# Performance work log

Hardware: AMD Instinct MI355X
Metric: run time of the kernel (lower is better)

Reference implementation:

```python
import jax, jax.numpy as jnp
import numpy as np

DIM = 64
B_GRAPHS = 16
N_NODES = 4096
N_EDGES = 16384
SLOPE = 0.01  # PyTorch leaky_relu default negative slope


def lrelu(x):
    return jnp.where(x >= 0, x, SLOPE * x)


def setup_inputs() -> dict:
    key = jax.random.key(0)
    ks = jax.random.split(key, 16)
    d = DIM

    def rn(k, shape, scale=0.05):
        return jax.random.normal(k, shape, dtype=jnp.float32) * scale

    def z(*s):
        return jnp.zeros(s, jnp.float32)

    return {
        "x": jax.random.normal(ks[0], (N_NODES, 3), dtype=jnp.float32),
        "edge_attr": jax.random.normal(ks[1], (N_EDGES, 4), dtype=jnp.float32),
        "edge_index": jax.random.randint(ks[2], (2, N_EDGES), 0, N_NODES),
        "batch": jnp.sort(jax.random.randint(ks[3], (N_NODES,), 0, B_GRAPHS)),
        # lin0
        "W0": rn(ks[4], (3, d)), "b0": z(d),
        # edge MLP: Linear(4,d) -> LeakyReLU -> Linear(d, d*d)
        "We1": rn(ks[5], (4, d)), "be1": z(d),
        "We2": rn(ks[6], (d, d * d), 0.01), "be2": z(d * d),
        # NNConv root weight + bias
        "root": rn(ks[7], (d, d)), "conv_b": z(d),
        # GRU(d, d)  (PyTorch layout: [3d, in] / [3d, hid], gate order r,z,n)
        "Wih": rn(ks[8], (3 * d, d)), "Whh": rn(ks[9], (3 * d, d)),
        "bih": z(3 * d), "bhh": z(3 * d),
        # Set2Set LSTM(2d, d)  (gate order i,f,g,o)
        "lWih": rn(ks[10], (4 * d, 2 * d)), "lWhh": rn(ks[11], (4 * d, d)),
        "lbih": z(4 * d), "lbhh": z(4 * d),
        # lin_out: Linear(2d, 2)
        "Wout": rn(ks[12], (2 * d, 2)), "bout": z(2),
    }


def _forward(x, edge_attr, W0, b0, We1, be1, We2, be2, root, conv_b,
             Wih, Whh, bih, bhh, lWih, lWhh, lbih, lbhh, Wout, bout,
             edge_index, batch):
    d = DIM
    N = x.shape[0]
    E = edge_attr.shape[0]
    src, dst = edge_index[0], edge_index[1]  # messages flow src(j) -> dst(i)

    out = lrelu(x @ W0 + b0)  # [N, d]
    h = out                    # GRU hidden state (h = out.unsqueeze(0))

    # Edge-conditioned weights: constant across the 6 iterations, compute once.
    he = lrelu(edge_attr @ We1 + be1)          # [E, d]
    W_e = (he @ We2 + be2).reshape(E, d, d)    # [E, d, d]
    deg = jax.ops.segment_sum(jnp.ones((E,), jnp.float32), dst, num_segments=N)
    inv_deg = (1.0 / jnp.maximum(deg, 1.0))[:, None]  # mean aggr, clamp like PyG

    for _ in range(6):
        # NNConv: gather x_j, per-edge matmul, scatter-mean, plus root term
        msg = jnp.einsum('ed,edf->ef', out[src], W_e)            # [E, d]
        agg = jax.ops.segment_sum(msg, dst, num_segments=N) * inv_deg
        m = lrelu(agg + out @ root + conv_b)                     # [N, d]
        # GRU cell (single step, PyTorch gate order r, z, n)
        gi = m @ Wih.T + bih
        gh = h @ Whh.T + bhh
        i_r, i_z, i_n = jnp.split(gi, 3, axis=-1)
        h_r, h_z, h_n = jnp.split(gh, 3, axis=-1)
        r = jax.nn.sigmoid(i_r + h_r)
        zg = jax.nn.sigmoid(i_z + h_z)
        n = jnp.tanh(i_n + r * h_n)
        h = (1.0 - zg) * n + zg * h
        out = h

    # Set2Set pooling, processing_steps = 1
    Bg = B_GRAPHS
    q_star = jnp.zeros((Bg, 2 * d), jnp.float32)
    hl = jnp.zeros((Bg, d), jnp.float32)
    cl = jnp.zeros((Bg, d), jnp.float32)
    gates = q_star @ lWih.T + lbih + hl @ lWhh.T + lbhh
    gi_, gf_, gg_, go_ = jnp.split(gates, 4, axis=-1)
    cl = jax.nn.sigmoid(gf_) * cl + jax.nn.sigmoid(gi_) * jnp.tanh(gg_)
    q = jax.nn.sigmoid(go_) * jnp.tanh(cl)         # [Bg, d]
    e = jnp.sum(out * q[batch], axis=-1)           # [N]
    emax = jax.ops.segment_max(e, batch, num_segments=Bg)
    a = jnp.exp(e - emax[batch])
    asum = jax.ops.segment_sum(a, batch, num_segments=Bg)
    a = a / asum[batch]                            # per-graph softmax attention
    rpool = jax.ops.segment_sum(a[:, None] * out, batch, num_segments=Bg)
    q_star = jnp.concatenate([q, rpool], axis=-1)  # [Bg, 2d]

    return q_star @ Wout + bout                    # [Bg, 2]


def reference(x, edge_attr, edge_index, batch, W0, b0, We1, be1, We2, be2,
              root, conv_b, Wih, Whh, bih, bhh, lWih, lWhh, lbih, lbhh,
              Wout, bout):
    return _forward(x, edge_attr, W0, b0, We1, be1, We2, be2, root, conv_b,
                    Wih, Whh, bih, bhh, lWih, lWhh, lbih, lbhh, Wout, bout,
                    edge_index, batch)
```

## Files before the change

### kernel.cpp

```cpp
#include <hip/hip_runtime.h>
#include <cstddef>

#define NE 16384
#define NN 4096
#define BG 16
#define NT 16
#define ACH 8

__device__ __forceinline__ float lrelu(float v){ return v >= 0.f ? v : 0.01f*v; }
__device__ __forceinline__ float sigm(float v){ return 1.f/(1.f + expf(-v)); }

__global__ __launch_bounds__(256) void setup_kernel(
    const float* __restrict__ x, const float* __restrict__ ea,
    const int* __restrict__ ei,
    const float* __restrict__ W0, const float* __restrict__ b0,
    const float* __restrict__ We1, const float* __restrict__ be1,
    const float* __restrict__ Wih, const float* __restrict__ Whh,
    float* __restrict__ W8T,
    float* __restrict__ h, float* __restrict__ he,
    int* __restrict__ deg, int* __restrict__ cnt)
{
    int t = blockIdx.x*256 + threadIdx.x;
    {
        int e = t >> 6, f = t & 63;
        float v = be1[f];
        #pragma unroll
        for (int d = 0; d < 4; ++d) v += ea[e*4+d]*We1[d*64+f];
        he[t] = lrelu(v);
    }
    if (t < NN*64) {
        int n = t >> 6, f = t & 63;
        float v = b0[f];
        #pragma unroll
        for (int d = 0; d < 3; ++d) v += x[n*3+d]*W0[d*64+f];
        h[t] = lrelu(v);
    }
    if (t < 32768) {
        int k = t >> 9, g = (t >> 3) & 63, j = t & 7;
        float v = 0.f;
        if (j < 3)      v = Wih[(j*64+g)*64 + k];
        else if (j < 6) v = Whh[((j-3)*64+g)*64 + k];
        W8T[t] = v;
    }
    if (t < NE) {
        atomicAdd(&deg[ei[NE + t]], 1);
        atomicAdd(&cnt[ei[t]], 1);
    }
}

__global__ __launch_bounds__(256) void scan_inv_kernel(
    const int* __restrict__ cnt, int* __restrict__ offs,
    const int* __restrict__ deg, const int* __restrict__ batch,
    float* __restrict__ inv_deg, int* __restrict__ gstart, int* __restrict__ gend)
{
    __shared__ int ps[256];
    int t = threadIdx.x;
    int base = t*16;
    int loc[16];
    int s = 0;
    #pragma unroll
    for (int i = 0; i < 16; ++i) { loc[i] = s; s += cnt[base+i]; }
    ps[t] = s; __syncthreads();
    for (int off = 1; off < 256; off <<= 1) {
        int v = 0;
        if (t >= off) v = ps[t-off];
        __syncthreads();
        if (t >= off) ps[t] += v;
        __syncthreads();
    }
    int pre = (t == 0) ? 0 : ps[t-1];
    #pragma unroll
    for (int i = 0; i < 16; ++i) offs[base+i] = pre + loc[i];
    if (t == 255) offs[NN] = pre + s;

    for (int i = 0; i < 16; ++i) {
        int n = base + i;
        inv_deg[n] = 1.f / fmaxf((float)deg[n], 1.f);
        int b  = batch[n];
        int bp = (n == 0)    ? -1 : batch[n-1];
        int bn = (n == NN-1) ? BG : batch[n+1];
        for (int g = bp+1; g <= b; ++g) gstart[g] = n;
        for (int g = b;   g <  bn; ++g) gend[g]   = n+1;
        if (n == 0)    for (int g = 0;   g < b;  ++g) gend[g]   = 0;
        if (n == NN-1) for (int g = b+1; g < BG; ++g) gstart[g] = NN;
    }
}

__global__ __launch_bounds__(256) void scatter_kernel(
    const int* __restrict__ ei, const int* __restrict__ offs,
    int* __restrict__ cnt,
    int* __restrict__ srcs, int* __restrict__ dsts, int* __restrict__ perm)
{
    int e = blockIdx.x*256 + threadIdx.x;
    if (e >= NE) return;
    int s = ei[e], d = ei[NE + e];
    int old = atomicSub(&cnt[s], 1);
    int pos = offs[s] + old - 1;
    srcs[pos] = s; dsts[pos] = d; perm[pos] = e;
}

__global__ __launch_bounds__(256) void reorder_kernel(
    const float* __restrict__ he, const int* __restrict__ perm,
    float* __restrict__ he_srt)
{
    int t = blockIdx.x*256 + threadIdx.x;
    he_srt[t] = he[(size_t)perm[t>>6]*64 + (t & 63)];
}

__global__ __launch_bounds__(1024) void conv_kernel(
    const float* __restrict__ h, const float* __restrict__ We2,
    const float* __restrict__ be2, const float* __restrict__ he_srt,
    const int* __restrict__ offs, const int* __restrict__ srcs,
    const int* __restrict__ dsts, float* __restrict__ agg)
{
    __shared__ float hsT[64][NT];
    __shared__ float Tb [NT][64];
    __shared__ float Tc [2][ACH][NT][64];
    __shared__ float he_s[2][128][ACH];
    int t  = threadIdx.x;
    int n0 = blockIdx.x * NT;

    { int n = t >> 6, i = t & 63; hsT[i][n] = h[(size_t)(n0+n)*64 + i]; }
    int ebase = offs[n0];
    int ecnt  = offs[n0+NT] - ebase;
    int eend  = ebase + ecnt;
    __syncthreads();

    int aT = t >> 6;
    int nT = ((t >> 4) & 3) * 4;
    int fT = (t & 15) * 4;
    int ct   = t - 512;
    int slot = ct >> 4;
    int f4   = (ct & 15) * 4;
    int nl0=-1,dt0=0,nl1=-1,dt1=0,nl2=-1,dt2=0,nl3=-1,dt3=0;
    float4 m0={0,0,0,0},m1={0,0,0,0},m2={0,0,0,0},m3={0,0,0,0};
    if (t >= 512) {
        if (slot      < ecnt) { nl0 = srcs[ebase+slot]    - n0; dt0 = dsts[ebase+slot];    }
        if (slot + 32 < ecnt) { nl1 = srcs[ebase+slot+32] - n0; dt1 = dsts[ebase+slot+32]; }
        if (slot + 64 < ecnt) { nl2 = srcs[ebase+slot+64] - n0; dt2 = dsts[ebase+slot+64]; }
        if (slot + 96 < ecnt) { nl3 = srcs[ebase+slot+96] - n0; dt3 = dsts[ebase+slot+96]; }
    }

#define EDGE_ACC(mj, nlj, row, buf_) \
    if (nlj >= 0) { \
        float4 hA = *(const float4*)&he_s[buf_][row][0]; \
        float4 hB = *(const float4*)&he_s[buf_][row][4]; \
        float4 t0 = *(const float4*)&Tc[buf_][0][nlj][f4]; \
        float4 t1 = *(const float4*)&Tc[buf_][1][nlj][f4]; \
        float4 t2 = *(const float4*)&Tc[buf_][2][nlj][f4]; \
        float4 t3 = *(const float4*)&Tc[buf_][3][nlj][f4]; \
        float4 t4 = *(const float4*)&Tc[buf_][4][nlj][f4]; \
        float4 t5 = *(const float4*)&Tc[buf_][5][nlj][f4]; \
        float4 t6 = *(const float4*)&Tc[buf_][6][nlj][f4]; \
        float4 t7 = *(const float4*)&Tc[buf_][7][nlj][f4]; \
        mj.x += hA.x*t0.x+hA.y*t1.x+hA.z*t2.x+hA.w*t3.x+hB.x*t4.x+hB.y*t5.x+hB.z*t6.x+hB.w*t7.x; \
        mj.y += hA.x*t0.y+hA.y*t1.y+hA.z*t2.y+hA.w*t3.y+hB.x*t4.y+hB.y*t5.y+hB.z*t6.y+hB.w*t7.y; \
        mj.z += hA.x*t0.z+hA.y*t1.z+hA.z*t2.z+hA.w*t3.z+hB.x*t4.z+hB.y*t5.z+hB.z*t6.z+hB.w*t7.z; \
        mj.w += hA.x*t0.w+hA.y*t1.w+hA.z*t2.w+hA.w*t3.w+hB.x*t4.w+hB.y*t5.w+hB.z*t6.w+hB.w*t7.w; \
    }

#define CONSUME(cm) { \
    int buf_ = (cm) & 1; \
    EDGE_ACC(m0, nl0, (slot),      buf_) \
    EDGE_ACC(m1, nl1, (slot+32),   buf_) \
    EDGE_ACC(m2, nl2, (slot+64),   buf_) \
    EDGE_ACC(m3, nl3, (slot+96),   buf_) \
    for (int e = ebase + 128 + slot; e < eend; e += 32) { \
        int nl = srcs[e] - n0, dtv = dsts[e]; \
        const float* hep = he_srt + (size_t)e*64 + (cm)*ACH; \
        float4 pm = {0,0,0,0}; \
        _Pragma("unroll") \
        for (int a = 0; a < ACH; ++a) { \
            float hv = hep[a]; \
            float4 tv = *(const float4*)&Tc[buf_][a][nl][f4]; \
            pm.x += hv*tv.x; pm.y += hv*tv.y; pm.z += hv*tv.z; pm.w += hv*tv.w; \
        } \
        if ((cm) == 0) { \
            float4 b = *(const float4*)&Tb[nl][f4]; \
            pm.x += b.x; pm.y += b.y; pm.z += b.z; pm.w += b.w; \
        } \
        float* ap = agg + (size_t)dtv*64 + f4; \
        atomicAdd(ap+0, pm.x); atomicAdd(ap+1, pm.y); \
        atomicAdd(ap+2, pm.z); atomicAdd(ap+3, pm.w); \
    } \
}

    for (int c = 0; c < 8; ++c) {
        if (t < 512) {
            const float* Wp = We2 + (size_t)(c*ACH + aT)*4096 + fT;
            float4 A0={0,0,0,0},A1={0,0,0,0},A2={0,0,0,0},A3={0,0,0,0};
            #pragma unroll 8
            for (int i = 0; i < 64; ++i) {
                float4 w  = *(const float4*)(Wp + (size_t)i*64);
                float4 hv = *(const float4*)&hsT[i][nT];
                A0.x += hv.x*w.x; A0.y += hv.x*w.y; A0.z += hv.x*w.z; A0.w += hv.x*w.w;
                A1.x += hv.y*w.x; A1.y += hv.y*w.y; A1.z += hv.y*w.z; A1.w += hv.y*w.w;
                A2.x += hv.z*w.x; A2.y += hv.z*w.y; A2.z += hv.z*w.z; A2.w += hv.z*w.w;
                A3.x += hv.w*w.x; A3.y += hv.w*w.y; A3.z += hv.w*w.z; A3.w += hv.w*w.w;
            }
            int buf = c & 1;
            *(float4*)&Tc[buf][aT][nT+0][fT] = A0;
            *(float4*)&Tc[buf][aT][nT+1][fT] = A1;
            *(float4*)&Tc[buf][aT][nT+2][fT] = A2;
            *(float4*)&Tc[buf][aT][nT+3][fT] = A3;
        } else {
            {
                int le = ct >> 2, a2 = (ct & 3) * 2;
                if (ebase + le < NE)
                    *(float2*)&he_s[c&1][le][a2] =
                        *(const float2*)&he_srt[(size_t)(ebase+le)*64 + c*ACH + a2];
            }
            if (c == 0) {
                int n = ct >> 5, fp = (ct & 31) * 2;
                float t0 = 0.f, t1 = 0.f;
                #pragma unroll 8
                for (int i = 0; i < 64; ++i) {
                    float hv = hsT[i][n];
                    float2 b = *(const float2*)&be2[(size_t)i*64 + fp];
                    t0 += hv*b.x; t1 += hv*b.y;
                }
                Tb[n][fp]   = t0;
                Tb[n][fp+1] = t1;
            } else {
                CONSUME(c-1);
            }
        }
        __syncthreads();
    }
    if (t >= 512) {
        CONSUME(7);
        if (nl0 >= 0) {
            float4 b = *(const float4*)&Tb[nl0][f4];
            float* ap = agg + (size_t)dt0*64 + f4;
            atomicAdd(ap+0, m0.x+b.x); atomicAdd(ap+1, m0.y+b.y);
            atomicAdd(ap+2, m0.z+b.z); atomicAdd(ap+3, m0.w+b.w);
        }
        if (nl1 >= 0) {
            float4 b = *(const float4*)&Tb[nl1][f4];
            float* ap = agg + (size_t)dt1*64 + f4;
            atomicAdd(ap+0, m1.x+b.x); atomicAdd(ap+1, m1.y+b.y);
            atomicAdd(ap+2, m1.z+b.z); atomicAdd(ap+3, m1.w+b.w);
        }
        if (nl2 >= 0) {
            float4 b = *(const float4*)&Tb[nl2][f4];
            float* ap = agg + (size_t)dt2*64 + f4;
            atomicAdd(ap+0, m2.x+b.x); atomicAdd(ap+1, m2.y+b.y);
            atomicAdd(ap+2, m2.z+b.z); atomicAdd(ap+3, m2.w+b.w);
        }
        if (nl3 >= 0) {
            float4 b = *(const float4*)&Tb[nl3][f4];
            float* ap = agg + (size_t)dt3*64 + f4;
            atomicAdd(ap+0, m3.x+b.x); atomicAdd(ap+1, m3.y+b.y);
            atomicAdd(ap+2, m3.z+b.z); atomicAdd(ap+3, m3.w+b.w);
        }
    }
#undef CONSUME
#undef EDGE_ACC
}

__global__ __launch_bounds__(512) void node_kernel(
    const float* __restrict__ W8T, const float* __restrict__ root,
    const float* __restrict__ conv_b, const float* __restrict__ inv_deg,
    const float* __restrict__ bih, const float* __restrict__ bhh,
    float* __restrict__ h, float* __restrict__ agg)
{
    __shared__ float hs[8][64];
    __shared__ float ms[8][64];
    int t = threadIdx.x;
    int n = t >> 6, g = t & 63;
    int gn = blockIdx.x*8 + n;
    hs[n][g] = h[(size_t)gn*64 + g];
    __syncthreads();
    {
        size_t ix = (size_t)gn*64 + g;
        float v = agg[ix]*inv_deg[gn] + conv_b[g];
        agg[ix] = 0.f;
        #pragma unroll 8
        for (int k = 0; k < 64; ++k) v += hs[n][k]*root[k*64 + g];
        ms[n][g] = lrelu(v);
    }
    __syncthreads();

    float ir=0.f, iz=0.f, in_=0.f, hr=0.f, hz=0.f, hn=0.f;
    const float* Wp = W8T + (size_t)g*8;
    #pragma unroll 8
    for (int k = 0; k < 64; ++k) {
        float am = ms[n][k], ah = hs[n][k];
        float4 w0 = *(const float4*)(Wp + (size_t)k*512);
        float4 w1 = *(const float4*)(Wp + (size_t)k*512 + 4);
        ir  += am*w0.x; iz += am*w0.y; in_ += am*w0.z;
        hr  += ah*w0.w; hz += ah*w1.x; hn  += ah*w1.y;
    }
    float r  = sigm(ir + bih[g]      + hr + bhh[g]);
    float z  = sigm(iz + bih[64+g]   + hz + bhh[64+g]);
    float nn = tanhf(in_ + bih[128+g] + r*(hn + bhh[128+g]));
    h[(size_t)gn*64 + g] = (1.f - z)*nn + z*hs[n][g];
}

__device__ __forceinline__ float q_val(const float* lbih, const float* lbhh, int g)
{
    float gi = lbih[g]     + lbhh[g];
    float gg = lbih[128+g] + lbhh[128+g];
    float go = lbih[192+g] + lbhh[192+g];
    return sigm(go)*tanhf(sigm(gi)*tanhf(gg));
}

__global__ __launch_bounds__(1024) void pool_kernel(
    const float* __restrict__ h, float* __restrict__ e,
    const int* __restrict__ gstart, const int* __restrict__ gend,
    const float* __restrict__ lbih, const float* __restrict__ lbhh,
    const float* __restrict__ Wout, const float* __restrict__ bout,
    float* __restrict__ out)
{
    __shared__ float red[1024];
    __shared__ float qs[64];
    __shared__ float rp[64];
    __shared__ float sval;
    int g = blockIdx.x, t = threadIdx.x;
    int s = gstart[g], en = gend[g];

    if (t < 64) qs[t] = q_val(lbih, lbhh, t);
    __syncthreads();
    int w = t >> 6, f = t & 63;
    for (int n = s + w; n < en; n += 16) {
        float p = h[(size_t)n*64 + f]*qs[f];
        #pragma unroll
        for (int off = 32; off; off >>= 1) p += __shfl_xor(p, off);
        if (f == 0) e[n] = p;
    }
    __syncthreads();

    float mx = -1e30f;
    for (int n = s+t; n < en; n += 1024) mx = fmaxf(mx, e[n]);
    red[t] = mx; __syncthreads();
    for (int st = 512; st; st >>= 1) { if (t < st) red[t] = fmaxf(red[t], red[t+st]); __syncthreads(); }
    if (t == 0) sval = red[0];
    __syncthreads();
    float lmx = sval;
    __syncthreads();

    float sm = 0.f;
    for (int n = s+t; n < en; n += 1024) { float a = expf(e[n]-lmx); e[n] = a; sm += a; }
    red[t] = sm; __syncthreads();
    for (int st = 512; st; st >>= 1) { if (t < st) red[t] += red[t+st]; __syncthreads(); }
    if (t == 0) sval = (red[0] > 0.f) ? 1.f/red[0] : 0.f;
    __syncthreads();
    float inv_asum = sval;
    __syncthreads();

    float racc = 0.f;
    for (int n = s+w; n < en; n += 16) racc += e[n]*h[(size_t)n*64 + f];
    red[t] = racc; __syncthreads();
    if (w == 0) {
        float a = 0.f;
        #pragma unroll
        for (int i = 0; i < 16; ++i) a += red[i*64 + f];
        rp[f] = a*inv_asum;
    }
    __syncthreads();

    if (t < 64) {
        float qv = qs[t];
        float p0 = qv*Wout[t*2]   + rp[t]*Wout[(64+t)*2];
        float p1 = qv*Wout[t*2+1] + rp[t]*Wout[(64+t)*2+1];
        #pragma unroll
        for (int off = 32; off; off >>= 1) { p0 += __shfl_xor(p0, off); p1 += __shfl_xor(p1, off); }
        if (t == 0) { out[g*2] = p0 + bout[0]; out[g*2+1] = p1 + bout[1]; }
    }
}

extern "C" void kernel_launch(void* const* d_in, const int* in_sizes, int n_in,
                              void* d_out, int out_size, void* d_ws, size_t ws_size,
                              hipStream_t stream)
{
    const float* x      = (const float*)d_in[0];
    const float* ea     = (const float*)d_in[1];
    const int*   ei     = (const int*)  d_in[2];
    const int*   batch  = (const int*)  d_in[3];
    const float* W0     = (const float*)d_in[4];
    const float* b0     = (const float*)d_in[5];
    const float* We1    = (const float*)d_in[6];
    const float* be1    = (const float*)d_in[7];
    const float* We2    = (const float*)d_in[8];
    const float* be2    = (const float*)d_in[9];
    const float* root   = (const float*)d_in[10];
    const float* conv_b = (const float*)d_in[11];
    const float* Wih    = (const float*)d_in[12];
    const float* Whh    = (const float*)d_in[13];
    const float* bih    = (const float*)d_in[14];
    const float* bhh    = (const float*)d_in[15];
    const float* lbih   = (const float*)d_in[18];
    const float* lbhh   = (const float*)d_in[19];
    const float* Wout   = (const float*)d_in[20];
    const float* bout   = (const float*)d_in[21];
    float* out = (float*)d_out;

    float* W = (float*)d_ws;
    size_t off = 0;
    float* h       = W + off; off += (size_t)NN*64;
    float* he      = W + off; off += (size_t)NE*64;
    float* he_srt  = W + off; off += (size_t)NE*64;
    float* agg     = W + off; off += (size_t)NN*64;
    float* W8T     = W + off; off += 32768;
    float* inv_deg = W + off; off += NN;
    float* e       = W + off; off += NN;
    int*   deg     = (int*)(W + off); off += NN;
    int*   cnt     = (int*)(W + off); off += NN;
    int*   offs    = (int*)(W + off); off += NN+1;
    int*   srcs    = (int*)(W + off); off += NE;
    int*   dsts    = (int*)(W + off); off += NE;
    int*   perm    = (int*)(W + off); off += NE;
    int*   gstart  = (int*)(W + off); off += BG;
    int*   gend    = (int*)(W + off); off += BG;

    hipMemsetAsync(deg, 0, 2*NN*sizeof(int), stream);
    hipMemsetAsync(agg, 0, (size_t)NN*64*sizeof(float), stream);
    setup_kernel<<<4096, 256, 0, stream>>>(x, ea, ei, W0, b0, We1, be1, Wih, Whh,
                                           W8T, h, he, deg, cnt);
    scan_inv_kernel<<<1, 256, 0, stream>>>(cnt, offs, deg, batch,
                                           inv_deg, gstart, gend);
    scatter_kernel<<<64, 256, 0, stream>>>(ei, offs, cnt, srcs, dsts, perm);
    reorder_kernel<<<4096, 256, 0, stream>>>(he, perm, he_srt);

    for (int it = 0; it < 6; ++it) {
        conv_kernel<<<NN/NT, 1024, 0, stream>>>(h, We2, be2, he_srt,
                                                offs, srcs, dsts, agg);
        node_kernel<<<NN/8, 512, 0, stream>>>(W8T, root, conv_b,
                                              inv_deg, bih, bhh, h, agg);
    }

    pool_kernel<<<BG, 1024, 0, stream>>>(h, e, gstart, gend, lbih, lbhh,
                                         Wout, bout, out);
}
```

Baseline: 588.1 us.

## Fuse GRU node update into next conv launch with double-buffered aggregation

The per-node GRU update of iteration k now runs at the start of the conv kernel for iteration k+1, on the block's own nodes, reading from a separate double-buffered aggregation array. This removes five node-kernel launches and a reload of h from global memory. The edge-MLP hidden computation also moves into the reorder kernel, which computes it directly in sorted order and drops the intermediate he buffer. In exchange the aggregation workspace doubles in size, and the conv kernel's shared-memory tile is reused for the message values.

```diff
diff --git a/kernel.cpp b/kernel.cpp
--- a/kernel.cpp
+++ b/kernel.cpp
@@ -11,24 +11,14 @@
 __device__ __forceinline__ float sigm(float v){ return 1.f/(1.f + expf(-v)); }
 
 __global__ __launch_bounds__(256) void setup_kernel(
-    const float* __restrict__ x, const float* __restrict__ ea,
-    const int* __restrict__ ei,
+    const float* __restrict__ x, const int* __restrict__ ei,
     const float* __restrict__ W0, const float* __restrict__ b0,
-    const float* __restrict__ We1, const float* __restrict__ be1,
     const float* __restrict__ Wih, const float* __restrict__ Whh,
-    float* __restrict__ W8T,
-    float* __restrict__ h, float* __restrict__ he,
+    float* __restrict__ W8T, float* __restrict__ h,
     int* __restrict__ deg, int* __restrict__ cnt)
 {
     int t = blockIdx.x*256 + threadIdx.x;
     {
-        int e = t >> 6, f = t & 63;
-        float v = be1[f];
-        #pragma unroll
-        for (int d = 0; d < 4; ++d) v += ea[e*4+d]*We1[d*64+f];
-        he[t] = lrelu(v);
-    }
-    if (t < NN*64) {
         int n = t >> 6, f = t & 63;
         float v = b0[f];
         #pragma unroll
@@ -100,23 +90,35 @@
 }
 
 __global__ __launch_bounds__(256) void reorder_kernel(
-    const float* __restrict__ he, const int* __restrict__ perm,
+    const float* __restrict__ ea, const int* __restrict__ perm,
+    const float* __restrict__ We1, const float* __restrict__ be1,
     float* __restrict__ he_srt)
 {
     int t = blockIdx.x*256 + threadIdx.x;
-    he_srt[t] = he[(size_t)perm[t>>6]*64 + (t & 63)];
-}
-
-__global__ __launch_bounds__(1024) void conv_kernel(
-    const float* __restrict__ h, const float* __restrict__ We2,
+    int e = t >> 6, f = t & 63;
+    int pe = perm[e];
+    float v = be1[f];
+    #pragma unroll
+    for (int d = 0; d < 4; ++d) v += ea[pe*4+d]*We1[d*64+f];
+    he_srt[t] = lrelu(v);
+}
+
+__global__ __launch_bounds__(1024) void conv_fused(
+    float* __restrict__ h, const float* __restrict__ We2,
     const float* __restrict__ be2, const float* __restrict__ he_srt,
     const int* __restrict__ offs, const int* __restrict__ srcs,
-    const int* __restrict__ dsts, float* __restrict__ agg)
+    const int* __restrict__ dsts, float* __restrict__ agg_cur,
+    float* __restrict__ agg_prev,
+    const float* __restrict__ W8T, const float* __restrict__ root,
+    const float* __restrict__ conv_b, const float* __restrict__ inv_deg,
+    const float* __restrict__ bih, const float* __restrict__ bhh,
+    int do_node)
 {
     __shared__ float hsT[64][NT];
     __shared__ float Tb [NT][64];
     __shared__ float Tc [2][ACH][NT][64];
     __shared__ float he_s[2][128][ACH];
+    float* ms = &Tc[0][0][0][0];
     int t  = threadIdx.x;
     int n0 = blockIdx.x * NT;
 
@@ -125,6 +127,38 @@
     int ecnt  = offs[n0+NT] - ebase;
     int eend  = ebase + ecnt;
     __syncthreads();
+
+    if (do_node) {
+        int n = t >> 6, g = t & 63;
+        int gn = n0 + n;
+        size_t ix = (size_t)gn*64 + g;
+        float v = agg_prev[ix]*inv_deg[gn] + conv_b[g];
+        agg_prev[ix] = 0.f;
+        #pragma unroll 8
+        for (int k = 0; k < 64; ++k) v += hsT[k][n]*root[k*64 + g];
+        ms[n*64 + g] = lrelu(v);
+        __syncthreads();
+
+        float ir=0.f, iz=0.f, in_=0.f, hr=0.f, hz=0.f, hn=0.f;
+        const float* Wp = W8T + (size_t)g*8;
+        #pragma unroll 8
+        for (int k = 0; k < 64; ++k) {
+            float am = ms[n*64 + k], ah = hsT[k][n];
+            float4 w0 = *(const float4*)(Wp + (size_t)k*512);
+            float4 w1 = *(const float4*)(Wp + (size_t)k*512 + 4);
+            ir  += am*w0.x; iz += am*w0.y; in_ += am*w0.z;
+            hr  += ah*w0.w; hz += ah*w1.x; hn  += ah*w1.y;
+        }
+        float r  = sigm(ir + bih[g]      + hr + bhh[g]);
+        float z  = sigm(iz + bih[64+g]   + hz + bhh[64+g]);
+        float nn = tanhf(in_ + bih[128+g] + r*(hn + bhh[128+g]));
+        float ho = hsT[g][n];
+        float hnew = (1.f - z)*nn + z*ho;
+        __syncthreads();
+        hsT[g][n] = hnew;
+        h[ix] = hnew;
+        __syncthreads();
+    }
 
     int aT = t >> 6;
     int nT = ((t >> 4) & 3) * 4;
@@ -179,7 +213,7 @@
             float4 b = *(const float4*)&Tb[nl][f4]; \
             pm.x += b.x; pm.y += b.y; pm.z += b.z; pm.w += b.w; \
         } \
-        float* ap = agg + (size_t)dtv*64 + f4; \
+        float* ap = agg_cur + (size_t)dtv*64 + f4; \
         atomicAdd(ap+0, pm.x); atomicAdd(ap+1, pm.y); \
         atomicAdd(ap+2, pm.z); atomicAdd(ap+3, pm.w); \
     } \
@@ -231,25 +265,25 @@
         CONSUME(7);
         if (nl0 >= 0) {
             float4 b = *(const float4*)&Tb[nl0][f4];
-            float* ap = agg + (size_t)dt0*64 + f4;
+            float* ap = agg_cur + (size_t)dt0*64 + f4;
             atomicAdd(ap+0, m0.x+b.x); atomicAdd(ap+1, m0.y+b.y);
             atomicAdd(ap+2, m0.z+b.z); atomicAdd(ap+3, m0.w+b.w);
         }
         if (nl1 >= 0) {
             float4 b = *(const float4*)&Tb[nl1][f4];
-            float* ap = agg + (size_t)dt1*64 + f4;
+            float* ap = agg_cur + (size_t)dt1*64 + f4;
             atomicAdd(ap+0, m1.x+b.x); atomicAdd(ap+1, m1.y+b.y);
             atomicAdd(ap+2, m1.z+b.z); atomicAdd(ap+3, m1.w+b.w);
         }
         if (nl2 >= 0) {
             float4 b = *(const float4*)&Tb[nl2][f4];
-            float* ap = agg + (size_t)dt2*64 + f4;
+            float* ap = agg_cur + (size_t)dt2*64 + f4;
             atomicAdd(ap+0, m2.x+b.x); atomicAdd(ap+1, m2.y+b.y);
             atomicAdd(ap+2, m2.z+b.z); atomicAdd(ap+3, m2.w+b.w);
         }
         if (nl3 >= 0) {
             float4 b = *(const float4*)&Tb[nl3][f4];
-            float* ap = agg + (size_t)dt3*64 + f4;
+            float* ap = agg_cur + (size_t)dt3*64 + f4;
             atomicAdd(ap+0, m3.x+b.x); atomicAdd(ap+1, m3.y+b.y);
             atomicAdd(ap+2, m3.z+b.z); atomicAdd(ap+3, m3.w+b.w);
         }
@@ -274,7 +308,6 @@
     {
         size_t ix = (size_t)gn*64 + g;
         float v = agg[ix]*inv_deg[gn] + conv_b[g];
-        agg[ix] = 0.f;
         #pragma unroll 8
         for (int k = 0; k < 64; ++k) v += hs[n][k]*root[k*64 + g];
         ms[n][g] = lrelu(v);
@@ -398,9 +431,8 @@
     float* W = (float*)d_ws;
     size_t off = 0;
     float* h       = W + off; off += (size_t)NN*64;
-    float* he      = W + off; off += (size_t)NE*64;
     float* he_srt  = W + off; off += (size_t)NE*64;
-    float* agg     = W + off; off += (size_t)NN*64;
+    float* agg     = W + off; off += (size_t)2*NN*64;
     float* W8T     = W + off; off += 32768;
     float* inv_deg = W + off; off += NN;
     float* e       = W + off; off += NN;
@@ -414,20 +446,24 @@
     int*   gend    = (int*)(W + off); off += BG;
 
     hipMemsetAsync(deg, 0, 2*NN*sizeof(int), stream);
-    hipMemsetAsync(agg, 0, (size_t)NN*64*sizeof(float), stream);
-    setup_kernel<<<4096, 256, 0, stream>>>(x, ea, ei, W0, b0, We1, be1, Wih, Whh,
-                                           W8T, h, he, deg, cnt);
+    hipMemsetAsync(agg, 0, (size_t)2*NN*64*sizeof(float), stream);
+    setup_kernel<<<1024, 256, 0, stream>>>(x, ei, W0, b0, Wih, Whh,
+                                           W8T, h, deg, cnt);
     scan_inv_kernel<<<1, 256, 0, stream>>>(cnt, offs, deg, batch,
                                            inv_deg, gstart, gend);
     scatter_kernel<<<64, 256, 0, stream>>>(ei, offs, cnt, srcs, dsts, perm);
-    reorder_kernel<<<4096, 256, 0, stream>>>(he, perm, he_srt);
+    reorder_kernel<<<4096, 256, 0, stream>>>(ea, perm, We1, be1, he_srt);
 
     for (int it = 0; it < 6; ++it) {
-        conv_kernel<<<NN/NT, 1024, 0, stream>>>(h, We2, be2, he_srt,
-                                                offs, srcs, dsts, agg);
-        node_kernel<<<NN/8, 512, 0, stream>>>(W8T, root, conv_b,
-                                              inv_deg, bih, bhh, h, agg);
-    }
+        float* agg_cur  = agg + (size_t)(it & 1) * NN * 64;
+        float* agg_prev = agg + (size_t)((it + 1) & 1) * NN * 64;
+        conv_fused<<<NN/NT, 1024, 0, stream>>>(h, We2, be2, he_srt,
+                                               offs, srcs, dsts, agg_cur, agg_prev,
+                                               W8T, root, conv_b, inv_deg,
+                                               bih, bhh, it > 0 ? 1 : 0);
+    }
+    node_kernel<<<NN/8, 512, 0, stream>>>(W8T, root, conv_b, inv_deg,
+                                          bih, bhh, h, agg + (size_t)NN*64);
 
     pool_kernel<<<BG, 1024, 0, stream>>>(h, e, gstart, gend, lbih, lbhh,
                                          Wout, bout, out);
```

Result: no change. 579.4 us (-1.5%).
